# Kernel optimization log

Hardware: AMD Instinct MI355X
Metric: run time of the kernel (lower is better)

Reference implementation:

```python
import jax, jax.numpy as jnp
import numpy as np

N_CLASS = 50257
EMB = 1024
HID = 1024
BATCH = 1024  # must equal HID due to the module's [H,H] zero state init
SEQ = 128


def setup_inputs() -> dict:
    key = jax.random.key(0)
    ks = jax.random.split(key, 8)
    s_e = 1.0 / np.sqrt(EMB)
    s_h = 1.0 / np.sqrt(HID)
    X = jax.random.randint(ks[0], (BATCH, SEQ), 0, N_CLASS, dtype=jnp.int32)
    C = jax.random.normal(ks[1], (N_CLASS, EMB), dtype=jnp.float32)
    # gate order along last axis: i, f, g, o (each block of size HID)
    Wx = jax.random.uniform(ks[2], (EMB, 4 * HID), jnp.float32, -s_e, s_e)
    bx = jax.random.uniform(ks[3], (4 * HID,), jnp.float32, -s_e, s_e)
    Wh = jax.random.uniform(ks[4], (HID, 4 * HID), jnp.float32, -s_h, s_h)
    bh = jax.random.uniform(ks[5], (4 * HID,), jnp.float32, -s_h, s_h)
    W_out = jax.random.uniform(ks[6], (HID, N_CLASS), jnp.float32, -s_h, s_h)
    b_out = jnp.ones((N_CLASS,), dtype=jnp.float32)  # nn.Parameter(torch.ones)
    return {"X": X, "C": C, "Wx": Wx, "bx": bx, "Wh": Wh, "bh": bh,
            "W_out": W_out, "b_out": b_out}


def _lstm_last_hidden(xs, Wx, bx, Wh, bh):
    # xs: [S, B, E]; with zero-initialized h/c of shape [H,H] and B == H,
    # the original broadcast-buggy code reduces to a standard LSTM.
    x_proj = jnp.einsum('sbe,eg->sbg', xs, Wx) + bx  # [S, B, 4H]
    B = xs.shape[1]
    H = Wh.shape[0]
    h0 = jnp.zeros((B, H), dtype=xs.dtype)
    c0 = jnp.zeros((B, H), dtype=xs.dtype)

    def step(carry, xp):
        h, c = carry
        gates = xp + h @ Wh + bh  # [B, 4H]
        i, f, g, o = jnp.split(gates, 4, axis=-1)
        i = jax.nn.sigmoid(i)
        f = jax.nn.sigmoid(f)
        g = jnp.tanh(g)
        o = jax.nn.sigmoid(o)
        c = f * c + i * g
        h = o * jnp.tanh(c)
        return (h, c), None

    (h, _), _ = jax.lax.scan(step, (h0, c0), x_proj)
    return h  # [B, H] last timestep hidden


def reference(X, C, Wx, bx, Wh, bh, W_out, b_out):
    emb = C[X]                      # [B, S, E]
    xs = jnp.swapaxes(emb, 0, 1)    # [S, B, E]  (transpose(0,1))
    h_last = _lstm_last_hidden(xs, Wx, bx, Wh, bh)
    return h_last @ W_out + b_out   # [B, n_class]
```

## Files before the change

kernel.cpp:

```cpp
#include <hip/hip_runtime.h>
#include <hip/hip_bf16.h>

#define SEQ_   128
#define NCLS_  50257
#define EMB_   1024
#define HID_   1024
#define BATCH_ 1024
#define G4_    4096

typedef __attribute__((ext_vector_type(8))) short short8;
typedef __attribute__((ext_vector_type(4))) float f32x4;

__device__ __forceinline__ void async_copy16(void* lds, const void* g) {
  __builtin_amdgcn_global_load_lds(
      (const __attribute__((address_space(1))) void*)g,
      (__attribute__((address_space(3))) void*)lds, 16, 0, 0);
}

__device__ __forceinline__ void mfma_acc(f32x4& c, const short8& a, const short8& b) {
  asm("v_mfma_f32_16x16x32_bf16 %0, %1, %2, %0" : "+v"(c) : "v"(a), "v"(b));
}

__device__ __forceinline__ float sigmoidf_(float x) {
  return 1.f / (1.f + __expf(-x));
}
__device__ __forceinline__ float tanhf_(float x) {
  x = fminf(12.f, fmaxf(-12.f, x));
  float e = __expf(2.f * x);
  return (e - 1.f) / (e + 1.f);
}
__device__ __forceinline__ float bf2f_(ushort u) {
  return __uint_as_float(((unsigned int)u) << 16);
}

template <int EPI>
__global__ __launch_bounds__(256) void gemm_bt(
    const __hip_bfloat16* __restrict__ A, const __hip_bfloat16* __restrict__ Bt,
    float* __restrict__ outF, __hip_bfloat16* __restrict__ outB,
    int Mreal, int Nreal, int K, long ostride,
    const float* __restrict__ bias0) {
  __shared__ __align__(16) char smem[65536];

  const int tid = threadIdx.x;
  const int lane = tid & 63;
  const int w = tid >> 6;
  const int wm = w >> 1;
  const int wn = w & 1;
  const int m0 = blockIdx.y * 128;
  const int n0 = blockIdx.x * 128;

  const int fr = lane & 15;
  const int kb = (lane >> 4) * 16;
  const int swz = (fr & 7) << 4;

  f32x4 acc[4][4];
#pragma unroll
  for (int i = 0; i < 4; ++i)
#pragma unroll
    for (int j = 0; j < 4; ++j) acc[i][j] = (f32x4)(0.0f);

  auto STAGE = [&](int kc, int b) {
#pragma unroll
    for (int q = 0; q < 8; ++q) {
      const int ridx = (q & 3) * 256 + tid;
      const int row = ridx >> 3;
      const int ch = ridx & 7;
      const __hip_bfloat16* src;
      char* dst;
      if (q < 4) {
        long ar = m0 + row; if (ar >= Mreal) ar = Mreal - 1;
        src = A + ar * (long)K + kc * 64 + ch * 8;
        dst = smem + b * 16384 + ridx * 16;
      } else {
        long br = n0 + row; if (br >= Nreal) br = Nreal - 1;
        src = Bt + br * (long)K + kc * 64 + ch * 8;
        dst = smem + 32768 + b * 16384 + ridx * 16;
      }
      async_copy16(dst, src);
    }
  };

  const int KC = K >> 6;
  STAGE(0, 0);
  for (int kc = 0; kc < KC; ++kc) {
    const int b = kc & 1;
    if (kc + 1 < KC) {
      STAGE(kc + 1, b ^ 1);
      asm volatile("s_waitcnt vmcnt(8)" ::: "memory");
    } else {
      asm volatile("s_waitcnt vmcnt(0)" ::: "memory");
    }
    __builtin_amdgcn_s_barrier();
    __builtin_amdgcn_sched_barrier(0);

    short8 aR[2][4], bR[2][4];
#pragma unroll
    for (int kk = 0; kk < 2; ++kk)
#pragma unroll
      for (int f = 0; f < 4; ++f) {
        aR[kk][f] = *(const short8*)(smem + b * 16384 +
                     (wm * 64 + f * 16 + fr) * 128 + ((kk * 64 + kb) ^ swz));
        bR[kk][f] = *(const short8*)(smem + 32768 + b * 16384 +
                     (wn * 64 + f * 16 + fr) * 128 + ((kk * 64 + kb) ^ swz));
      }
#pragma unroll
    for (int fm = 0; fm < 4; ++fm)
#pragma unroll
      for (int fn = 0; fn < 4; ++fn) {
        mfma_acc(acc[fm][fn], aR[0][fm], bR[0][fn]);
        mfma_acc(acc[fm][fn], aR[1][fm], bR[1][fn]);
      }
    __builtin_amdgcn_sched_barrier(0);
    __builtin_amdgcn_s_barrier();
  }

  const int cn = lane & 15;
  const int rb = (lane >> 4) * 4;
#pragma unroll
  for (int fn = 0; fn < 4; ++fn) {
    const int col = n0 + wn * 64 + fn * 16 + cn;
    const float badd = (col < Nreal) ? bias0[col] : 0.f;
#pragma unroll
    for (int fm = 0; fm < 4; ++fm) {
#pragma unroll
      for (int r = 0; r < 4; ++r) {
        const int row = m0 + wm * 64 + fm * 16 + rb + r;
        const float v = acc[fm][fn][r] + badd;
        if (EPI == 0) {
          if (row < Mreal) outB[(long)row * ostride + col] = __float2bfloat16(v);
        } else {
          if (col < Nreal && row < Mreal) outF[(long)row * ostride + col] = v;
        }
      }
    }
  }
}

__global__ __launch_bounds__(512) void lstm_step(
    const __hip_bfloat16* __restrict__ hprev,
    const __hip_bfloat16* __restrict__ Whs,
    const __hip_bfloat16* __restrict__ Epr,
    const int* __restrict__ X,
    float* __restrict__ cbuf,
    __hip_bfloat16* __restrict__ hnext,
    __hip_bfloat16* __restrict__ hfin,
    int t, int last) {
  extern __shared__ __align__(16) char smem[];
  float* gacc = (float*)smem;

  const int tid = threadIdx.x;
  const int lane = tid & 63;
  const int w = tid >> 6;
  const int wm = (w >> 1) & 1;
  const int wn = w & 1;
  const int kh = w >> 2;
  const int bid = blockIdx.x;
  const int xcd = bid & 7;
  const int j = bid >> 3;
  const int ht = xcd * 4 + (j & 3);
  const int mt = j >> 2;
  const int m0 = mt * 128;
  const int h0 = ht * 32;

  const int fr = lane & 15;
  const int kb = (lane >> 4) * 16;
  const int swz = (fr & 7) << 4;

  const int crow = tid >> 2;
  const int hq = tid & 3;
  const int prow = m0 + crow;
  const int tok1 = X[prow * SEQ_ + t];
  ushort4 ep[8];
  float cold[8];
#pragma unroll
  for (int jj = 0; jj < 8; ++jj) {
    ep[jj] = *(const ushort4*)(Epr + (size_t)tok1 * G4_ + (h0 + hq * 8 + jj) * 4);
    cold[jj] = cbuf[(size_t)prow * HID_ + h0 + hq * 8 + jj];
  }

  f32x4 acc[4][4];
#pragma unroll
  for (int i = 0; i < 4; ++i)
#pragma unroll
    for (int g = 0; g < 4; ++g) acc[i][g] = (f32x4)(0.0f);

  auto STAGE = [&](int kc, int b) {
#pragma unroll
    for (int q = 0; q < 8; ++q) {
      const int region = q >> 1;
      const int r = (q & 1) * 512 + tid;
      const int row = r >> 3;
      const int ch = r & 7;
      const __hip_bfloat16* src;
      if (region < 2) {
        src = hprev + (size_t)(m0 + row) * HID_ + region * 512 + kc * 64 + ch * 8;
      } else {
        const int g = row >> 5, hh = row & 31;
        src = Whs + (size_t)(g * 1024 + h0 + hh) * HID_ + (region - 2) * 512 +
              kc * 64 + ch * 8;
      }
      async_copy16(smem + region * 32768 + b * 16384 + r * 16, src);
    }
  };

  STAGE(0, 0);
  for (int kc = 0; kc < 8; ++kc) {
    const int b = kc & 1;
    if (kc < 7) {
      STAGE(kc + 1, b ^ 1);
      asm volatile("s_waitcnt vmcnt(8)" ::: "memory");
    } else {
      asm volatile("s_waitcnt vmcnt(0)" ::: "memory");
    }
    __builtin_amdgcn_s_barrier();
    __builtin_amdgcn_sched_barrier(0);

    const char* baseA = smem + kh * 32768 + b * 16384;
    const char* baseB = smem + 65536 + kh * 32768 + b * 16384;
    short8 aR[2][4], bR[2][4];
#pragma unroll
    for (int kk = 0; kk < 2; ++kk)
#pragma unroll
      for (int f = 0; f < 4; ++f) {
        aR[kk][f] = *(const short8*)(baseA + (wm * 64 + f * 16 + fr) * 128 +
                                     ((kk * 64 + kb) ^ swz));
        bR[kk][f] = *(const short8*)(baseB + (f * 32 + wn * 16 + fr) * 128 +
                                     ((kk * 64 + kb) ^ swz));
      }
#pragma unroll
    for (int fm = 0; fm < 4; ++fm)
#pragma unroll
      for (int g = 0; g < 4; ++g) {
        mfma_acc(acc[fm][g], aR[0][fm], bR[0][g]);
        mfma_acc(acc[fm][g], aR[1][fm], bR[1][g]);
      }
    __builtin_amdgcn_sched_barrier(0);
    __builtin_amdgcn_s_barrier();
  }

  const int cn = lane & 15;
  const int rb = (lane >> 4) * 4;
  if (kh == 0) {
#pragma unroll
    for (int fm = 0; fm < 4; ++fm)
#pragma unroll
      for (int g = 0; g < 4; ++g)
#pragma unroll
        for (int r = 0; r < 4; ++r)
          gacc[(wm * 64 + fm * 16 + rb + r) * 132 + (wn * 16 + cn) * 4 + g] =
              acc[fm][g][r];
  }
  __syncthreads();
  if (kh == 1) {
#pragma unroll
    for (int fm = 0; fm < 4; ++fm)
#pragma unroll
      for (int g = 0; g < 4; ++g)
#pragma unroll
        for (int r = 0; r < 4; ++r)
          gacc[(wm * 64 + fm * 16 + rb + r) * 132 + (wn * 16 + cn) * 4 + g] +=
              acc[fm][g][r];
  }
  __syncthreads();

  const float* gr = gacc + crow * 132 + hq * 32;
  f32x4 cnew0, cnew1;
  short8 hv;
#pragma unroll
  for (int jj = 0; jj < 8; ++jj) {
    const f32x4 g4 = *(const f32x4*)(gr + jj * 4);
    const float iv = sigmoidf_(g4[0] + bf2f_(ep[jj].x));
    const float fv = sigmoidf_(g4[1] + bf2f_(ep[jj].y));
    const float gv = tanhf_(g4[2] + bf2f_(ep[jj].z));
    const float ov = sigmoidf_(g4[3] + bf2f_(ep[jj].w));
    const float cv = fv * cold[jj] + iv * gv;
    if (jj < 4) cnew0[jj] = cv; else cnew1[jj - 4] = cv;
    const float hval = ov * tanhf_(cv);
    const __hip_bfloat16 hb = __float2bfloat16(hval);
    hv[jj] = *reinterpret_cast<const short*>(&hb);
  }
  float* cdst = cbuf + (size_t)prow * HID_ + h0 + hq * 8;
  *(f32x4*)cdst = cnew0;
  *(f32x4*)(cdst + 4) = cnew1;
  const int hcolb = h0 + hq * 8;
  const int hswb = (hcolb & ~63) | ((hcolb & 63) ^ ((prow & 7) << 3));
  *(short8*)(hnext + (size_t)prow * HID_ + hswb) = hv;
  if (last) *(short8*)(hfin + (size_t)prow * HID_ + hswb) = hv;
}

template <bool SWZ>
__global__ __launch_bounds__(256) void conv_bf16_k(const float* __restrict__ in,
                                                   __hip_bfloat16* __restrict__ out, int n4) {
  const int i = blockIdx.x * 256 + threadIdx.x;
  if (i >= n4) return;
  const float4 v = ((const float4*)in)[i];
  int o = i * 4;
  if (SWZ) {
    const int row = o >> 10, col = o & 1023;
    const int cs = (col & ~63) | ((col & 63) ^ ((row & 7) << 3));
    o = (o & ~1023) | cs;
  }
  out[o + 0] = __float2bfloat16(v.x);
  out[o + 1] = __float2bfloat16(v.y);
  out[o + 2] = __float2bfloat16(v.z);
  out[o + 3] = __float2bfloat16(v.w);
}

template <bool PERM, bool SWZ>
__global__ __launch_bounds__(256) void transpose_conv(const float* __restrict__ in,
                                                      __hip_bfloat16* __restrict__ out,
                                                      int R, int C) {
  __shared__ float tile[32][33];
  const int c0 = blockIdx.x * 32, r0 = blockIdx.y * 32;
  const int tx = threadIdx.x, ty = threadIdx.y;
#pragma unroll
  for (int i = 0; i < 4; ++i) {
    const int r = r0 + ty + i * 8, cc = c0 + tx;
    tile[ty + i * 8][tx] = (r < R && cc < C) ? in[(size_t)r * C + cc] : 0.f;
  }
  __syncthreads();
#pragma unroll
  for (int i = 0; i < 4; ++i) {
    const int ro = c0 + ty + i * 8, co = r0 + tx;
    if (ro < C && co < R) {
      const int n = PERM ? ((ro & 1023) * 4 + (ro >> 10)) : ro;
      int k = co;
      if (SWZ) k = (k & ~63) | ((k & 63) ^ ((n & 7) << 3));
      out[(size_t)n * R + k] = __float2bfloat16(tile[tx][ty + i * 8]);
    }
  }
}

__global__ __launch_bounds__(256) void bias_perm(const float* __restrict__ bx,
                                                 const float* __restrict__ bh,
                                                 float* __restrict__ bP) {
  const int n = blockIdx.x * 256 + threadIdx.x;
  if (n >= G4_) return;
  const int h = n >> 2, g = n & 3;
  bP[n] = bx[g * HID_ + h] + bh[g * HID_ + h];
}

extern "C" void kernel_launch(void* const* d_in, const int* in_sizes, int n_in,
                              void* d_out, int out_size, void* d_ws, size_t ws_size,
                              hipStream_t stream) {
  const int* X = (const int*)d_in[0];
  const float* C = (const float*)d_in[1];
  const float* Wx = (const float*)d_in[2];
  const float* bx = (const float*)d_in[3];
  const float* Wh = (const float*)d_in[4];
  const float* bh = (const float*)d_in[5];
  const float* Wo = (const float*)d_in[6];
  const float* bo = (const float*)d_in[7];
  float* out = (float*)d_out;

  char* p = (char*)d_ws;
  const size_t szCb  = (size_t)NCLS_ * EMB_ * 2;
  const size_t szWxt = (size_t)G4_ * EMB_ * 2;
  const size_t szWhs = (size_t)G4_ * HID_ * 2;
  const size_t szEpr = (size_t)NCLS_ * G4_ * 2;
  const size_t szH   = (size_t)BATCH_ * HID_ * 2;
  const size_t szC   = (size_t)BATCH_ * HID_ * 4;
  const size_t szBp  = (size_t)G4_ * 4;
  if (ws_size < szCb + szWxt + szWhs + szEpr + 3 * szH + szC + szBp) return;

  __hip_bfloat16* Cb   = (__hip_bfloat16*)p; p += szCb;
  __hip_bfloat16* WxtP = (__hip_bfloat16*)p; p += szWxt;
  __hip_bfloat16* Whs  = (__hip_bfloat16*)p; p += szWhs;
  __hip_bfloat16* Epr  = (__hip_bfloat16*)p; p += szEpr;
  __hip_bfloat16* hA   = (__hip_bfloat16*)p; p += szH;
  __hip_bfloat16* hB   = (__hip_bfloat16*)p; p += szH;
  __hip_bfloat16* hfin = (__hip_bfloat16*)p; p += szH;
  float* cbuf          = (float*)p;          p += szC;
  float* bP            = (float*)p;          p += szBp;

  {
    const int n4 = NCLS_ * EMB_ / 4;
    conv_bf16_k<true><<<(n4 + 255) / 256, 256, 0, stream>>>(C, Cb, n4);
  }
  transpose_conv<true, true><<<dim3(G4_ / 32, EMB_ / 32), dim3(32, 8), 0, stream>>>(
      Wx, WxtP, EMB_, G4_);
  transpose_conv<false, true><<<dim3(G4_ / 32, HID_ / 32), dim3(32, 8), 0, stream>>>(
      Wh, Whs, HID_, G4_);
  bias_perm<<<G4_ / 256, 256, 0, stream>>>(bx, bh, bP);

  gemm_bt<0><<<dim3(G4_ / 128, (NCLS_ + 127) / 128), 256, 0, stream>>>(
      Cb, WxtP, nullptr, Epr, NCLS_, G4_, EMB_, G4_, bP);

  hipMemsetAsync(hA, 0, szH, stream);
  hipMemsetAsync(cbuf, 0, szC, stream);

  for (int t = 0; t < SEQ_; ++t) {
    const __hip_bfloat16* hp = (t & 1) ? hB : hA;
    __hip_bfloat16* hn = (t & 1) ? hA : hB;
    lstm_step<<<256, 512, 131072, stream>>>(hp, Whs, Epr, X, cbuf, hn, hfin, t,
                                            (int)(t == SEQ_ - 1));
  }

  __hip_bfloat16* Wot = Cb;
  transpose_conv<false, true><<<dim3((NCLS_ + 31) / 32, HID_ / 32), dim3(32, 8), 0,
                                stream>>>(Wo, Wot, HID_, NCLS_);

  gemm_bt<2><<<dim3((NCLS_ + 127) / 128, BATCH_ / 128), 256, 0, stream>>>(
      hfin, Wot, out, nullptr, BATCH_, NCLS_, HID_, NCLS_, bo);
}
```

Baseline: 3.306 ms.

## Fuse LSTM time steps into one persistent cooperative kernel with stripe barriers

Replaces the 128 per-timestep lstm_step launches with one cooperative kernel that loops over time. Each block keeps its cell state in registers instead of reading and writing a global c buffer. Blocks that share a 128-row batch stripe synchronize through an atomic counter and spin-wait between steps. This removes per-launch overhead and cell-state memory traffic, at the cost of spin-barrier latency and reliance on all 256 blocks being co-resident.

```diff
diff --git a/kernel.cpp b/kernel.cpp
--- a/kernel.cpp
+++ b/kernel.cpp
@@ -136,15 +136,12 @@
   }
 }
 
-__global__ __launch_bounds__(512) void lstm_step(
-    const __hip_bfloat16* __restrict__ hprev,
+__global__ __launch_bounds__(512) void lstm_all(
     const __hip_bfloat16* __restrict__ Whs,
     const __hip_bfloat16* __restrict__ Epr,
     const int* __restrict__ X,
-    float* __restrict__ cbuf,
-    __hip_bfloat16* __restrict__ hnext,
-    __hip_bfloat16* __restrict__ hfin,
-    int t, int last) {
+    __hip_bfloat16* __restrict__ hbuf,
+    int* __restrict__ bar) {
   extern __shared__ __align__(16) char smem[];
   float* gacc = (float*)smem;
 
@@ -155,137 +152,152 @@
   const int wn = w & 1;
   const int kh = w >> 2;
   const int bid = blockIdx.x;
-  const int xcd = bid & 7;
-  const int j = bid >> 3;
-  const int ht = xcd * 4 + (j & 3);
-  const int mt = j >> 2;
-  const int m0 = mt * 128;
-  const int h0 = ht * 32;
+  const int stripe = bid >> 5;
+  const int slice = bid & 31;
+  const int m0 = stripe * 128;
+  const int h0 = slice * 32;
 
   const int fr = lane & 15;
   const int kb = (lane >> 4) * 16;
   const int swz = (fr & 7) << 4;
+  const int cn = lane & 15;
+  const int rb = (lane >> 4) * 4;
 
   const int crow = tid >> 2;
   const int hq = tid & 3;
   const int prow = m0 + crow;
-  const int tok1 = X[prow * SEQ_ + t];
-  ushort4 ep[8];
-  float cold[8];
-#pragma unroll
-  for (int jj = 0; jj < 8; ++jj) {
-    ep[jj] = *(const ushort4*)(Epr + (size_t)tok1 * G4_ + (h0 + hq * 8 + jj) * 4);
-    cold[jj] = cbuf[(size_t)prow * HID_ + h0 + hq * 8 + jj];
-  }
-
-  f32x4 acc[4][4];
-#pragma unroll
-  for (int i = 0; i < 4; ++i)
-#pragma unroll
-    for (int g = 0; g < 4; ++g) acc[i][g] = (f32x4)(0.0f);
-
-  auto STAGE = [&](int kc, int b) {
-#pragma unroll
-    for (int q = 0; q < 8; ++q) {
-      const int region = q >> 1;
-      const int r = (q & 1) * 512 + tid;
-      const int row = r >> 3;
-      const int ch = r & 7;
-      const __hip_bfloat16* src;
-      if (region < 2) {
-        src = hprev + (size_t)(m0 + row) * HID_ + region * 512 + kc * 64 + ch * 8;
+
+  float cst[8];
+#pragma unroll
+  for (int jj = 0; jj < 8; ++jj) cst[jj] = 0.f;
+
+#pragma unroll 1
+  for (int t = 0; t < SEQ_; ++t) {
+    const __hip_bfloat16* hcur = hbuf + (size_t)(t & 1) * (1024 * 1024);
+    __hip_bfloat16* hnxt = hbuf + (size_t)((t + 1) & 1) * (1024 * 1024);
+
+    const int tok1 = X[prow * SEQ_ + t];
+
+    f32x4 acc[4][4];
+#pragma unroll
+    for (int i = 0; i < 4; ++i)
+#pragma unroll
+      for (int g = 0; g < 4; ++g) acc[i][g] = (f32x4)(0.0f);
+
+    auto STAGE = [&](int kc, int b) {
+#pragma unroll
+      for (int q = 0; q < 8; ++q) {
+        const int region = q >> 1;
+        const int r = (q & 1) * 512 + tid;
+        const int row = r >> 3;
+        const int ch = r & 7;
+        const __hip_bfloat16* src;
+        if (region < 2) {
+          src = hcur + (size_t)(m0 + row) * HID_ + region * 512 + kc * 64 + ch * 8;
+        } else {
+          const int g = row >> 5, hh = row & 31;
+          src = Whs + (size_t)(g * 1024 + h0 + hh) * HID_ + (region - 2) * 512 +
+                kc * 64 + ch * 8;
+        }
+        async_copy16(smem + region * 32768 + b * 16384 + r * 16, src);
+      }
+    };
+
+    STAGE(0, 0);
+
+    ushort4 ep[8];
+#pragma unroll
+    for (int jj = 0; jj < 8; ++jj)
+      ep[jj] = *(const ushort4*)(Epr + (size_t)tok1 * G4_ + (h0 + hq * 8 + jj) * 4);
+
+    for (int kc = 0; kc < 8; ++kc) {
+      const int b = kc & 1;
+      if (kc < 7) {
+        STAGE(kc + 1, b ^ 1);
+        asm volatile("s_waitcnt vmcnt(8)" ::: "memory");
       } else {
-        const int g = row >> 5, hh = row & 31;
-        src = Whs + (size_t)(g * 1024 + h0 + hh) * HID_ + (region - 2) * 512 +
-              kc * 64 + ch * 8;
-      }
-      async_copy16(smem + region * 32768 + b * 16384 + r * 16, src);
-    }
-  };
-
-  STAGE(0, 0);
-  for (int kc = 0; kc < 8; ++kc) {
-    const int b = kc & 1;
-    if (kc < 7) {
-      STAGE(kc + 1, b ^ 1);
-      asm volatile("s_waitcnt vmcnt(8)" ::: "memory");
-    } else {
-      asm volatile("s_waitcnt vmcnt(0)" ::: "memory");
-    }
-    __builtin_amdgcn_s_barrier();
-    __builtin_amdgcn_sched_barrier(0);
-
-    const char* baseA = smem + kh * 32768 + b * 16384;
-    const char* baseB = smem + 65536 + kh * 32768 + b * 16384;
-    short8 aR[2][4], bR[2][4];
-#pragma unroll
-    for (int kk = 0; kk < 2; ++kk)
-#pragma unroll
-      for (int f = 0; f < 4; ++f) {
-        aR[kk][f] = *(const short8*)(baseA + (wm * 64 + f * 16 + fr) * 128 +
-                                     ((kk * 64 + kb) ^ swz));
-        bR[kk][f] = *(const short8*)(baseB + (f * 32 + wn * 16 + fr) * 128 +
-                                     ((kk * 64 + kb) ^ swz));
-      }
-#pragma unroll
-    for (int fm = 0; fm < 4; ++fm)
-#pragma unroll
-      for (int g = 0; g < 4; ++g) {
-        mfma_acc(acc[fm][g], aR[0][fm], bR[0][g]);
-        mfma_acc(acc[fm][g], aR[1][fm], bR[1][g]);
-      }
-    __builtin_amdgcn_sched_barrier(0);
-    __builtin_amdgcn_s_barrier();
-  }
-
-  const int cn = lane & 15;
-  const int rb = (lane >> 4) * 4;
-  if (kh == 0) {
-#pragma unroll
-    for (int fm = 0; fm < 4; ++fm)
-#pragma unroll
-      for (int g = 0; g < 4; ++g)
-#pragma unroll
-        for (int r = 0; r < 4; ++r)
-          gacc[(wm * 64 + fm * 16 + rb + r) * 132 + (wn * 16 + cn) * 4 + g] =
-              acc[fm][g][r];
-  }
-  __syncthreads();
-  if (kh == 1) {
-#pragma unroll
-    for (int fm = 0; fm < 4; ++fm)
-#pragma unroll
-      for (int g = 0; g < 4; ++g)
-#pragma unroll
-        for (int r = 0; r < 4; ++r)
-          gacc[(wm * 64 + fm * 16 + rb + r) * 132 + (wn * 16 + cn) * 4 + g] +=
-              acc[fm][g][r];
-  }
-  __syncthreads();
-
-  const float* gr = gacc + crow * 132 + hq * 32;
-  f32x4 cnew0, cnew1;
-  short8 hv;
-#pragma unroll
-  for (int jj = 0; jj < 8; ++jj) {
-    const f32x4 g4 = *(const f32x4*)(gr + jj * 4);
-    const float iv = sigmoidf_(g4[0] + bf2f_(ep[jj].x));
-    const float fv = sigmoidf_(g4[1] + bf2f_(ep[jj].y));
-    const float gv = tanhf_(g4[2] + bf2f_(ep[jj].z));
-    const float ov = sigmoidf_(g4[3] + bf2f_(ep[jj].w));
-    const float cv = fv * cold[jj] + iv * gv;
-    if (jj < 4) cnew0[jj] = cv; else cnew1[jj - 4] = cv;
-    const float hval = ov * tanhf_(cv);
-    const __hip_bfloat16 hb = __float2bfloat16(hval);
-    hv[jj] = *reinterpret_cast<const short*>(&hb);
-  }
-  float* cdst = cbuf + (size_t)prow * HID_ + h0 + hq * 8;
-  *(f32x4*)cdst = cnew0;
-  *(f32x4*)(cdst + 4) = cnew1;
-  const int hcolb = h0 + hq * 8;
-  const int hswb = (hcolb & ~63) | ((hcolb & 63) ^ ((prow & 7) << 3));
-  *(short8*)(hnext + (size_t)prow * HID_ + hswb) = hv;
-  if (last) *(short8*)(hfin + (size_t)prow * HID_ + hswb) = hv;
+        asm volatile("s_waitcnt vmcnt(0)" ::: "memory");
+      }
+      __builtin_amdgcn_s_barrier();
+      __builtin_amdgcn_sched_barrier(0);
+
+      const char* baseA = smem + kh * 32768 + b * 16384;
+      const char* baseB = smem + 65536 + kh * 32768 + b * 16384;
+      short8 aR[2][4], bR[2][4];
+#pragma unroll
+      for (int kk = 0; kk < 2; ++kk)
+#pragma unroll
+        for (int f = 0; f < 4; ++f) {
+          aR[kk][f] = *(const short8*)(baseA + (wm * 64 + f * 16 + fr) * 128 +
+                                       ((kk * 64 + kb) ^ swz));
+          bR[kk][f] = *(const short8*)(baseB + (f * 32 + wn * 16 + fr) * 128 +
+                                       ((kk * 64 + kb) ^ swz));
+        }
+#pragma unroll
+      for (int fm = 0; fm < 4; ++fm)
+#pragma unroll
+        for (int g = 0; g < 4; ++g) {
+          mfma_acc(acc[fm][g], aR[0][fm], bR[0][g]);
+          mfma_acc(acc[fm][g], aR[1][fm], bR[1][g]);
+        }
+      __builtin_amdgcn_sched_barrier(0);
+      __builtin_amdgcn_s_barrier();
+    }
+
+    if (kh == 0) {
+#pragma unroll
+      for (int fm = 0; fm < 4; ++fm)
+#pragma unroll
+        for (int g = 0; g < 4; ++g)
+#pragma unroll
+          for (int r = 0; r < 4; ++r)
+            gacc[(wm * 64 + fm * 16 + rb + r) * 132 + (wn * 16 + cn) * 4 + g] =
+                acc[fm][g][r];
+    }
+    __syncthreads();
+    if (kh == 1) {
+#pragma unroll
+      for (int fm = 0; fm < 4; ++fm)
+#pragma unroll
+        for (int g = 0; g < 4; ++g)
+#pragma unroll
+          for (int r = 0; r < 4; ++r)
+            gacc[(wm * 64 + fm * 16 + rb + r) * 132 + (wn * 16 + cn) * 4 + g] +=
+                acc[fm][g][r];
+    }
+    __syncthreads();
+
+    const float* gr = gacc + crow * 132 + hq * 32;
+    short8 hv;
+#pragma unroll
+    for (int jj = 0; jj < 8; ++jj) {
+      const f32x4 g4 = *(const f32x4*)(gr + jj * 4);
+      const float iv = sigmoidf_(g4[0] + bf2f_(ep[jj].x));
+      const float fv = sigmoidf_(g4[1] + bf2f_(ep[jj].y));
+      const float gv = tanhf_(g4[2] + bf2f_(ep[jj].z));
+      const float ov = sigmoidf_(g4[3] + bf2f_(ep[jj].w));
+      const float cv = fv * cst[jj] + iv * gv;
+      cst[jj] = cv;
+      const float hval = ov * tanhf_(cv);
+      const __hip_bfloat16 hb = __float2bfloat16(hval);
+      hv[jj] = *reinterpret_cast<const short*>(&hb);
+    }
+    const int hcolb = h0 + hq * 8;
+    const int hswb = (hcolb & ~63) | ((hcolb & 63) ^ ((prow & 7) << 3));
+    *(short8*)(hnxt + (size_t)prow * HID_ + hswb) = hv;
+
+    __syncthreads();
+    if (tid == 0) {
+      __builtin_amdgcn_fence(__ATOMIC_RELEASE, "agent");
+      atomicAdd(&bar[stripe], 1);
+      const int target = 32 * (t + 1);
+      while (__hip_atomic_load(&bar[stripe], __ATOMIC_RELAXED,
+                               __HIP_MEMORY_SCOPE_AGENT) < target)
+        __builtin_amdgcn_s_sleep(2);
+      __builtin_amdgcn_fence(__ATOMIC_ACQUIRE, "agent");
+    }
+    __syncthreads();
+  }
 }
 
 template <bool SWZ>
@@ -358,20 +370,18 @@
   const size_t szWxt = (size_t)G4_ * EMB_ * 2;
   const size_t szWhs = (size_t)G4_ * HID_ * 2;
   const size_t szEpr = (size_t)NCLS_ * G4_ * 2;
-  const size_t szH   = (size_t)BATCH_ * HID_ * 2;
-  const size_t szC   = (size_t)BATCH_ * HID_ * 4;
+  const size_t szHb  = (size_t)2 * BATCH_ * HID_ * 2;
   const size_t szBp  = (size_t)G4_ * 4;
-  if (ws_size < szCb + szWxt + szWhs + szEpr + 3 * szH + szC + szBp) return;
+  const size_t szBar = 128;
+  if (ws_size < szCb + szWxt + szWhs + szEpr + szHb + szBp + szBar) return;
 
   __hip_bfloat16* Cb   = (__hip_bfloat16*)p; p += szCb;
   __hip_bfloat16* WxtP = (__hip_bfloat16*)p; p += szWxt;
   __hip_bfloat16* Whs  = (__hip_bfloat16*)p; p += szWhs;
   __hip_bfloat16* Epr  = (__hip_bfloat16*)p; p += szEpr;
-  __hip_bfloat16* hA   = (__hip_bfloat16*)p; p += szH;
-  __hip_bfloat16* hB   = (__hip_bfloat16*)p; p += szH;
-  __hip_bfloat16* hfin = (__hip_bfloat16*)p; p += szH;
-  float* cbuf          = (float*)p;          p += szC;
+  __hip_bfloat16* hbuf = (__hip_bfloat16*)p; p += szHb;
   float* bP            = (float*)p;          p += szBp;
+  int* bar             = (int*)p;            p += szBar;
 
   {
     const int n4 = NCLS_ * EMB_ / 4;
@@ -386,14 +396,13 @@
   gemm_bt<0><<<dim3(G4_ / 128, (NCLS_ + 127) / 128), 256, 0, stream>>>(
       Cb, WxtP, nullptr, Epr, NCLS_, G4_, EMB_, G4_, bP);
 
-  hipMemsetAsync(hA, 0, szH, stream);
-  hipMemsetAsync(cbuf, 0, szC, stream);
-
-  for (int t = 0; t < SEQ_; ++t) {
-    const __hip_bfloat16* hp = (t & 1) ? hB : hA;
-    __hip_bfloat16* hn = (t & 1) ? hA : hB;
-    lstm_step<<<256, 512, 131072, stream>>>(hp, Whs, Epr, X, cbuf, hn, hfin, t,
-                                            (int)(t == SEQ_ - 1));
+  hipMemsetAsync(hbuf, 0, (size_t)BATCH_ * HID_ * 2, stream);
+  hipMemsetAsync(bar, 0, szBar, stream);
+
+  {
+    void* kargs[] = {(void*)&Whs, (void*)&Epr, (void*)&X, (void*)&hbuf, (void*)&bar};
+    hipLaunchCooperativeKernel((void*)lstm_all, dim3(256), dim3(512), kargs,
+                               131072, stream);
   }
 
   __hip_bfloat16* Wot = Cb;
@@ -401,5 +410,5 @@
                                 stream>>>(Wo, Wot, HID_, NCLS_);
 
   gemm_bt<2><<<dim3((NCLS_ + 127) / 128, BATCH_ / 128), 256, 0, stream>>>(
-      hfin, Wot, out, nullptr, BATCH_, NCLS_, HID_, NCLS_, bo);
-}
+      hbuf, Wot, out, nullptr, BATCH_, NCLS_, HID_, NCLS_, bo);
+}
```

Measured after the change: 4.786 ms. 1.45x slower.

## Prepack Wh into MFMA fragment order and load B directly into registers

Applied to the files above, without the earlier changes.

Wh is pre-packed once into per-lane MFMA B-fragment order, so each LSTM step kernel loads its B operand straight from global into registers with coalesced 16-byte loads. This removes the LDS staging and LDS reads for the weight. Only the hidden-state A tile still goes through LDS, now with a three-buffer ring and a two-stage prefetch. The change also lowers LDS to 96KB, adds launch_bounds(512,2), and raises MFMA priority with setprio. In exchange it costs more VGPRs for the double-buffered B fragments, and the waitcnt accounting becomes more fragile.

```diff
diff --git a/kernel.cpp b/kernel.cpp
--- a/kernel.cpp
+++ b/kernel.cpp
@@ -136,9 +136,31 @@
   }
 }
 
-__global__ __launch_bounds__(512) void lstm_step(
+__global__ __launch_bounds__(256) void pack_b(const float* __restrict__ Wh,
+                                              __hip_bfloat16* __restrict__ Bpk) {
+  const int gtid = blockIdx.x * 256 + threadIdx.x;
+  const int l = gtid & 63;
+  const int tile = gtid >> 6;
+  const int g = tile & 3;
+  const int kk = (tile >> 2) & 1;
+  const int kc = (tile >> 3) & 7;
+  const int kh = (tile >> 6) & 1;
+  const int wn = (tile >> 7) & 1;
+  const int ht = tile >> 8;
+  const int h = ht * 32 + wn * 16 + (l & 15);
+  const int k0 = kh * 512 + kc * 64 + kk * 32 + (l >> 4) * 8;
+  short8 v;
+#pragma unroll
+  for (int e = 0; e < 8; ++e) {
+    const __hip_bfloat16 b = __float2bfloat16(Wh[(size_t)(k0 + e) * G4_ + g * 1024 + h]);
+    v[e] = *reinterpret_cast<const short*>(&b);
+  }
+  *(short8*)(Bpk + (size_t)gtid * 8) = v;
+}
+
+__global__ __launch_bounds__(512, 2) void lstm_step(
     const __hip_bfloat16* __restrict__ hprev,
-    const __hip_bfloat16* __restrict__ Whs,
+    const __hip_bfloat16* __restrict__ Bpk,
     const __hip_bfloat16* __restrict__ Epr,
     const int* __restrict__ X,
     float* __restrict__ cbuf,
@@ -165,11 +187,81 @@
   const int fr = lane & 15;
   const int kb = (lane >> 4) * 16;
   const int swz = (fr & 7) << 4;
+  const int cn = lane & 15;
+  const int rb = (lane >> 4) * 4;
 
   const int crow = tid >> 2;
   const int hq = tid & 3;
   const int prow = m0 + crow;
   const int tok1 = X[prow * SEQ_ + t];
+
+  const __hip_bfloat16* bb =
+      Bpk + (size_t)(((ht * 2 + wn) * 2 + kh) * 64) * 512 + lane * 8;
+
+  f32x4 acc[4][4];
+#pragma unroll
+  for (int i = 0; i < 4; ++i)
+#pragma unroll
+    for (int g = 0; g < 4; ++g) acc[i][g] = (f32x4)(0.0f);
+
+  auto STAGE_A = [&](int kc, int b) {
+#pragma unroll
+    for (int q = 0; q < 4; ++q) {
+      const int region = q >> 1;
+      const int r = (q & 1) * 512 + tid;
+      const int row = r >> 3, ch = r & 7;
+      const __hip_bfloat16* src =
+          hprev + (size_t)(m0 + row) * HID_ + region * 512 + kc * 64 + ch * 8;
+      async_copy16(smem + b * 32768 + region * 16384 + r * 16, src);
+    }
+  };
+
+  short8 bR[2][2][4];
+
+  STAGE_A(0, 0);
+#pragma unroll
+  for (int kk = 0; kk < 2; ++kk)
+#pragma unroll
+    for (int g = 0; g < 4; ++g)
+      bR[0][kk][g] = *(const short8*)(bb + (0 * 8 + kk * 4 + g) * 512);
+  STAGE_A(1, 1);
+
+#pragma unroll
+  for (int kc = 0; kc < 8; ++kc) {
+    __builtin_amdgcn_s_barrier();
+    if (kc + 1 < 8) {
+#pragma unroll
+      for (int kk = 0; kk < 2; ++kk)
+#pragma unroll
+        for (int g = 0; g < 4; ++g)
+          bR[(kc + 1) & 1][kk][g] =
+              *(const short8*)(bb + ((kc + 1) * 8 + kk * 4 + g) * 512);
+    }
+    if (kc + 2 < 8) STAGE_A(kc + 2, (kc + 2) % 3);
+    if (kc < 6)      asm volatile("s_waitcnt vmcnt(24)" ::: "memory");
+    else if (kc == 6) asm volatile("s_waitcnt vmcnt(20)" ::: "memory");
+    else             asm volatile("s_waitcnt vmcnt(8)" ::: "memory");
+    __builtin_amdgcn_sched_barrier(0);
+
+    const char* baseA = smem + (kc % 3) * 32768 + kh * 16384;
+    short8 aR[2][4];
+#pragma unroll
+    for (int kk = 0; kk < 2; ++kk)
+#pragma unroll
+      for (int f = 0; f < 4; ++f)
+        aR[kk][f] = *(const short8*)(baseA + (wm * 64 + f * 16 + fr) * 128 +
+                                     ((kk * 64 + kb) ^ swz));
+    __builtin_amdgcn_s_setprio(1);
+#pragma unroll
+    for (int fm = 0; fm < 4; ++fm)
+#pragma unroll
+      for (int g = 0; g < 4; ++g) {
+        mfma_acc(acc[fm][g], aR[0][fm], bR[kc & 1][0][g]);
+        mfma_acc(acc[fm][g], aR[1][fm], bR[kc & 1][1][g]);
+      }
+    __builtin_amdgcn_s_setprio(0);
+  }
+
   ushort4 ep[8];
   float cold[8];
 #pragma unroll
@@ -178,68 +270,7 @@
     cold[jj] = cbuf[(size_t)prow * HID_ + h0 + hq * 8 + jj];
   }
 
-  f32x4 acc[4][4];
-#pragma unroll
-  for (int i = 0; i < 4; ++i)
-#pragma unroll
-    for (int g = 0; g < 4; ++g) acc[i][g] = (f32x4)(0.0f);
-
-  auto STAGE = [&](int kc, int b) {
-#pragma unroll
-    for (int q = 0; q < 8; ++q) {
-      const int region = q >> 1;
-      const int r = (q & 1) * 512 + tid;
-      const int row = r >> 3;
-      const int ch = r & 7;
-      const __hip_bfloat16* src;
-      if (region < 2) {
-        src = hprev + (size_t)(m0 + row) * HID_ + region * 512 + kc * 64 + ch * 8;
-      } else {
-        const int g = row >> 5, hh = row & 31;
-        src = Whs + (size_t)(g * 1024 + h0 + hh) * HID_ + (region - 2) * 512 +
-              kc * 64 + ch * 8;
-      }
-      async_copy16(smem + region * 32768 + b * 16384 + r * 16, src);
-    }
-  };
-
-  STAGE(0, 0);
-  for (int kc = 0; kc < 8; ++kc) {
-    const int b = kc & 1;
-    if (kc < 7) {
-      STAGE(kc + 1, b ^ 1);
-      asm volatile("s_waitcnt vmcnt(8)" ::: "memory");
-    } else {
-      asm volatile("s_waitcnt vmcnt(0)" ::: "memory");
-    }
-    __builtin_amdgcn_s_barrier();
-    __builtin_amdgcn_sched_barrier(0);
-
-    const char* baseA = smem + kh * 32768 + b * 16384;
-    const char* baseB = smem + 65536 + kh * 32768 + b * 16384;
-    short8 aR[2][4], bR[2][4];
-#pragma unroll
-    for (int kk = 0; kk < 2; ++kk)
-#pragma unroll
-      for (int f = 0; f < 4; ++f) {
-        aR[kk][f] = *(const short8*)(baseA + (wm * 64 + f * 16 + fr) * 128 +
-                                     ((kk * 64 + kb) ^ swz));
-        bR[kk][f] = *(const short8*)(baseB + (f * 32 + wn * 16 + fr) * 128 +
-                                     ((kk * 64 + kb) ^ swz));
-      }
-#pragma unroll
-    for (int fm = 0; fm < 4; ++fm)
-#pragma unroll
-      for (int g = 0; g < 4; ++g) {
-        mfma_acc(acc[fm][g], aR[0][fm], bR[0][g]);
-        mfma_acc(acc[fm][g], aR[1][fm], bR[1][g]);
-      }
-    __builtin_amdgcn_sched_barrier(0);
-    __builtin_amdgcn_s_barrier();
-  }
-
-  const int cn = lane & 15;
-  const int rb = (lane >> 4) * 4;
+  __syncthreads();
   if (kh == 0) {
 #pragma unroll
     for (int fm = 0; fm < 4; ++fm)
@@ -356,16 +387,16 @@
   char* p = (char*)d_ws;
   const size_t szCb  = (size_t)NCLS_ * EMB_ * 2;
   const size_t szWxt = (size_t)G4_ * EMB_ * 2;
-  const size_t szWhs = (size_t)G4_ * HID_ * 2;
+  const size_t szBpk = (size_t)G4_ * HID_ * 2;
   const size_t szEpr = (size_t)NCLS_ * G4_ * 2;
   const size_t szH   = (size_t)BATCH_ * HID_ * 2;
   const size_t szC   = (size_t)BATCH_ * HID_ * 4;
   const size_t szBp  = (size_t)G4_ * 4;
-  if (ws_size < szCb + szWxt + szWhs + szEpr + 3 * szH + szC + szBp) return;
+  if (ws_size < szCb + szWxt + szBpk + szEpr + 3 * szH + szC + szBp) return;
 
   __hip_bfloat16* Cb   = (__hip_bfloat16*)p; p += szCb;
   __hip_bfloat16* WxtP = (__hip_bfloat16*)p; p += szWxt;
-  __hip_bfloat16* Whs  = (__hip_bfloat16*)p; p += szWhs;
+  __hip_bfloat16* Bpk  = (__hip_bfloat16*)p; p += szBpk;
   __hip_bfloat16* Epr  = (__hip_bfloat16*)p; p += szEpr;
   __hip_bfloat16* hA   = (__hip_bfloat16*)p; p += szH;
   __hip_bfloat16* hB   = (__hip_bfloat16*)p; p += szH;
@@ -379,8 +410,7 @@
   }
   transpose_conv<true, true><<<dim3(G4_ / 32, EMB_ / 32), dim3(32, 8), 0, stream>>>(
       Wx, WxtP, EMB_, G4_);
-  transpose_conv<false, true><<<dim3(G4_ / 32, HID_ / 32), dim3(32, 8), 0, stream>>>(
-      Wh, Whs, HID_, G4_);
+  pack_b<<<2048, 256, 0, stream>>>(Wh, Bpk);
   bias_perm<<<G4_ / 256, 256, 0, stream>>>(bx, bh, bP);
 
   gemm_bt<0><<<dim3(G4_ / 128, (NCLS_ + 127) / 128), 256, 0, stream>>>(
@@ -392,8 +422,8 @@
   for (int t = 0; t < SEQ_; ++t) {
     const __hip_bfloat16* hp = (t & 1) ? hB : hA;
     __hip_bfloat16* hn = (t & 1) ? hA : hB;
-    lstm_step<<<256, 512, 131072, stream>>>(hp, Whs, Epr, X, cbuf, hn, hfin, t,
-                                            (int)(t == SEQ_ - 1));
+    lstm_step<<<256, 512, 98304, stream>>>(hp, Bpk, Epr, X, cbuf, hn, hfin, t,
+                                           (int)(t == SEQ_ - 1));
   }
 
   __hip_bfloat16* Wot = Cb;
```

New measurement: 3.162 ms. -4.4%, faster.
